# Kernel tuning notes

Hardware: AMD Instinct MI355X
Metric: run time of the kernel (lower is better)

Reference implementation:

```python
import jax, jax.numpy as jnp
import numpy as np

B, W, C, H = 2, 2048, 1024, 16
K = C // H  # 64
LN_EPS = 1e-5


def setup_inputs() -> dict:
    key = jax.random.key(0)
    ks = jax.random.split(key, 8)
    return {
        "seq1": jax.random.normal(ks[0], (B, W, C), jnp.float32),
        "seq2": jax.random.normal(ks[1], (B, W, C), jnp.float32),
        "ln_gamma": jnp.ones((C,), jnp.float32),
        "ln_beta": jnp.zeros((C,), jnp.float32),
        "q_proj": jax.random.normal(ks[2], (H, C, K), jnp.float32) * 0.02,
        "k_proj": jax.random.normal(ks[3], (H, C, K), jnp.float32) * 0.02,
        "v_proj": jax.random.normal(ks[4], (H, C, K), jnp.float32) * 0.02,
        "mixer_w": jax.random.normal(ks[5], (C, C), jnp.float32) * 0.02,
        "mixer_b": jnp.zeros((C,), jnp.float32),
    }


def _layernorm(x, gamma, beta):
    mu = jnp.mean(x, axis=-1, keepdims=True)
    var = jnp.mean(jnp.square(x - mu), axis=-1, keepdims=True)
    return (x - mu) * jax.lax.rsqrt(var + LN_EPS) * gamma + beta


def reference(seq1, seq2, ln_gamma, ln_beta, q_proj, k_proj, v_proj, mixer_w, mixer_b):
    x1 = _layernorm(seq1, ln_gamma, ln_beta)  # [B,W,C]
    x2 = _layernorm(seq2, ln_gamma, ln_beta)
    # per-head projections: [B,W,C] x [H,C,K] -> [B,H,W,K]
    q = jnp.einsum("bwc,hck->bhwk", x1, q_proj)
    k = jnp.einsum("bwc,hck->bhwk", x2, k_proj)
    v = jnp.einsum("bwc,hck->bhwk", x2, v_proj)
    scores = jnp.einsum("bhqk,bhmk->bhqm", q, k) / jnp.sqrt(jnp.float32(K))
    # causal mask (is_decoder=True)
    causal = jnp.tril(jnp.ones((W, W), bool))
    scores = jnp.where(causal[None, None], scores, jnp.float32(-jnp.inf))
    probs = jax.nn.softmax(scores, axis=-1)
    out = jnp.einsum("bhqm,bhmk->bhqk", probs, v)  # [B,H,W,K]
    out = out.transpose(0, 2, 1, 3).reshape(B, W, C)  # [B,W,C]
    return out @ mixer_w.T + mixer_b
```

## Files before the change

### kernel.cpp

```cpp
#include <hip/hip_runtime.h>
#include <math.h>

#define B_ 2
#define W_ 2048
#define C_ 1024
#define H_ 16
#define K_ 64
#define LN_EPS 1e-5f

typedef __attribute__((ext_vector_type(8))) short short8;
typedef __attribute__((ext_vector_type(4))) float float4v;

__device__ inline unsigned short f2bf(float f) {
  unsigned u = __float_as_uint(f);
  u += 0x7fffu + ((u >> 16) & 1u);
  return (unsigned short)(u >> 16);
}

__device__ __forceinline__ void gload_lds16(const short* g, short* l) {
  __builtin_amdgcn_global_load_lds(
      (const __attribute__((address_space(1))) void*)g,
      (__attribute__((address_space(3))) void*)l, 16, 0, 0);
}

__device__ inline float block_sum(float val) {
  __shared__ float sb[4];
  #pragma unroll
  for (int o = 32; o > 0; o >>= 1) val += __shfl_down(val, o, 64);
  int lane = threadIdx.x & 63, wid = threadIdx.x >> 6;
  if (lane == 0) sb[wid] = val;
  __syncthreads();
  float r = sb[0] + sb[1] + sb[2] + sb[3];
  __syncthreads();
  return r;
}

__global__ __launch_bounds__(256) void ln_kernel(
    const float* __restrict__ seq1, const float* __restrict__ seq2,
    const float* __restrict__ gamma, const float* __restrict__ beta,
    short* __restrict__ x1b, short* __restrict__ x2b) {
  int row = blockIdx.x;
  const int nrows = B_ * W_;
  bool first = row < nrows;
  const float* src = first ? seq1 : seq2;
  short* dst = first ? x1b : x2b;
  int r = first ? row : row - nrows;

  const float4* p = (const float4*)(src + (size_t)r * C_);
  float4 v = p[threadIdx.x];
  float mean = block_sum(v.x + v.y + v.z + v.w) * (1.0f / C_);
  float dx = v.x - mean, dy = v.y - mean, dz = v.z - mean, dw = v.w - mean;
  float var = block_sum(dx * dx + dy * dy + dz * dz + dw * dw) * (1.0f / C_);
  float rstd = rsqrtf(var + LN_EPS);

  float4 g = ((const float4*)gamma)[threadIdx.x];
  float4 b = ((const float4*)beta)[threadIdx.x];
  uint2 o;
  o.x = (unsigned)f2bf(dx * rstd * g.x + b.x) |
        ((unsigned)f2bf(dy * rstd * g.y + b.y) << 16);
  o.y = (unsigned)f2bf(dz * rstd * g.z + b.z) |
        ((unsigned)f2bf(dw * rstd * g.w + b.w) << 16);
  ((uint2*)(dst + (size_t)r * C_))[threadIdx.x] = o;
}

__global__ __launch_bounds__(256) void wprep_proj_kernel(
    const float* __restrict__ qp, const float* __restrict__ kp,
    const float* __restrict__ vp,
    short* __restrict__ wqt, short* __restrict__ wkt, short* __restrict__ wvt) {
  int cb = blockIdx.x, h = blockIdx.y, which = blockIdx.z;
  const float* P = (which == 0 ? qp : (which == 1 ? kp : vp)) + (size_t)h * C_ * K_;
  short* Wt = (which == 0 ? wqt : (which == 1 ? wkt : wvt));
  float scale = (which == 0) ? 0.125f : 1.0f;

  __shared__ float Ls[64][65];
  int t = threadIdx.x;
  {
    int cr = t >> 2, ks = (t & 3) * 16;
    const float* src = P + (size_t)(cb * 64 + cr) * K_ + ks;
    #pragma unroll
    for (int j = 0; j < 4; ++j) {
      float4 v = *(const float4*)(src + j * 4);
      Ls[cr][ks + j * 4 + 0] = v.x; Ls[cr][ks + j * 4 + 1] = v.y;
      Ls[cr][ks + j * 4 + 2] = v.z; Ls[cr][ks + j * 4 + 3] = v.w;
    }
  }
  __syncthreads();
  int kr = t >> 2, cs = (t & 3) * 16;
  unsigned u[8];
  #pragma unroll
  for (int i = 0; i < 8; ++i) {
    float a = Ls[cs + 2 * i][kr] * scale;
    float b = Ls[cs + 2 * i + 1][kr] * scale;
    u[i] = (unsigned)f2bf(a) | ((unsigned)f2bf(b) << 16);
  }
  short* dst = Wt + ((size_t)h * 64 + kr) * C_ + cb * 64 + cs;
  uint4 p0; p0.x = u[0]; p0.y = u[1]; p0.z = u[2]; p0.w = u[3];
  uint4 p1; p1.x = u[4]; p1.y = u[5]; p1.z = u[6]; p1.w = u[7];
  *(uint4*)dst = p0;
  *(uint4*)(dst + 8) = p1;
}

__global__ __launch_bounds__(256) void wprep_mix_kernel(
    const float* __restrict__ wm, short* __restrict__ wmb) {
  int gid = blockIdx.x * 256 + threadIdx.x;
  float4 v = ((const float4*)wm)[gid];
  uint2 o;
  o.x = (unsigned)f2bf(v.x) | ((unsigned)f2bf(v.y) << 16);
  o.y = (unsigned)f2bf(v.z) | ((unsigned)f2bf(v.w) << 16);
  ((uint2*)wmb)[gid] = o;
}

__device__ __forceinline__ void gemm_core(
    const short* __restrict__ A, const short* __restrict__ Bt,
    int arow0, int brow0, short* As, short* Bs, float4v acc[4][4]) {
  int tid = threadIdx.x;
  int wave = tid >> 6, lane = tid & 63;
  int lr = lane >> 3, lc = lane & 7;
  int sc = lc ^ lr;
  int wr = wave >> 1, wc = wave & 1;
  int lg = lane >> 4, ll = lane & 15;

  #pragma unroll
  for (int mi = 0; mi < 4; ++mi)
    #pragma unroll
    for (int ni = 0; ni < 4; ++ni) {
      acc[mi][ni][0] = 0.f; acc[mi][ni][1] = 0.f;
      acc[mi][ni][2] = 0.f; acc[mi][ni][3] = 0.f;
    }

  for (int k0 = 0; k0 < C_; k0 += 64) {
    __syncthreads();
    #pragma unroll
    for (int j = 0; j < 4; ++j) {
      int seg = wave * 4 + j;
      int r = seg * 8 + lr;
      gload_lds16(A + (size_t)(arow0 + r) * C_ + k0 + sc * 8, As + seg * 512);
      gload_lds16(Bt + (size_t)(brow0 + r) * C_ + k0 + sc * 8, Bs + seg * 512);
    }
    __syncthreads();
    #pragma unroll
    for (int kc = 0; kc < 2; ++kc) {
      int cc = kc * 4 + lg;
      short8 af[4], bf[4];
      #pragma unroll
      for (int mi = 0; mi < 4; ++mi) {
        int m = wr * 64 + mi * 16 + ll;
        af[mi] = *(const short8*)&As[m * 64 + ((cc ^ (m & 7)) << 3)];
      }
      #pragma unroll
      for (int ni = 0; ni < 4; ++ni) {
        int n = wc * 64 + ni * 16 + ll;
        bf[ni] = *(const short8*)&Bs[n * 64 + ((cc ^ (n & 7)) << 3)];
      }
      #pragma unroll
      for (int mi = 0; mi < 4; ++mi)
        #pragma unroll
        for (int ni = 0; ni < 4; ++ni)
          acc[mi][ni] = __builtin_amdgcn_mfma_f32_16x16x32_bf16(
              af[mi], bf[ni], acc[mi][ni], 0, 0, 0);
    }
  }
}

__global__ __launch_bounds__(256, 3) void gemm_qkv_kernel(
    const short* __restrict__ x1b, const short* __restrict__ x2b,
    const short* __restrict__ wqt, const short* __restrict__ wkt,
    const short* __restrict__ wvt,
    short* __restrict__ qb, short* __restrict__ kb, short* __restrict__ vtb) {
  __shared__ short As[128 * 64], Bs[128 * 64];
  int z = blockIdx.z;
  const short *A, *Bt;
  int arow0, brow0;
  if (z == 0)      { A = x1b; Bt = wqt; arow0 = blockIdx.x * 128; brow0 = blockIdx.y * 128; }
  else if (z == 1) { A = x2b; Bt = wkt; arow0 = blockIdx.x * 128; brow0 = blockIdx.y * 128; }
  else             { A = wvt; Bt = x2b; arow0 = blockIdx.y * 128; brow0 = blockIdx.x * 128; }

  float4v acc[4][4];
  gemm_core(A, Bt, arow0, brow0, As, Bs, acc);

  int wave = threadIdx.x >> 6, lane = threadIdx.x & 63;
  int wr = wave >> 1, wc = wave & 1, lg = lane >> 4, ll = lane & 15;
  if (z <= 1) {
    short* O = (z == 0) ? qb : kb;
    #pragma unroll
    for (int mi = 0; mi < 4; ++mi)
      #pragma unroll
      for (int ni = 0; ni < 4; ++ni) {
        int n = brow0 + wc * 64 + ni * 16 + ll;
        int h = n >> 6, kk = n & 63;
        #pragma unroll
        for (int r2 = 0; r2 < 4; ++r2) {
          int m = arow0 + wr * 64 + mi * 16 + lg * 4 + r2;
          int b = m >> 11, w = m & (W_ - 1);
          O[((size_t)(b * H_ + h) * W_ + w) * K_ + kk] = (short)f2bf(acc[mi][ni][r2]);
        }
      }
  } else {
    #pragma unroll
    for (int mi = 0; mi < 4; ++mi)
      #pragma unroll
      for (int ni = 0; ni < 4; ++ni) {
        int n = brow0 + wc * 64 + ni * 16 + ll;
        int b = n >> 11, w = n & (W_ - 1);
        #pragma unroll
        for (int r2 = 0; r2 < 4; ++r2) {
          int m = arow0 + wr * 64 + mi * 16 + lg * 4 + r2;
          int h = m >> 6, kk = m & 63;
          vtb[((size_t)(b * H_ + h) * K_ + kk) * W_ + w] = (short)f2bf(acc[mi][ni][r2]);
        }
      }
  }
}

__global__ __launch_bounds__(256, 3) void gemm_mix_kernel(
    const short* __restrict__ attnb, const short* __restrict__ wmb,
    const float* __restrict__ bias, float* __restrict__ out) {
  __shared__ short As[128 * 64], Bs[128 * 64];
  int arow0 = blockIdx.x * 128, brow0 = blockIdx.y * 128;
  float4v acc[4][4];
  gemm_core(attnb, wmb, arow0, brow0, As, Bs, acc);

  int wave = threadIdx.x >> 6, lane = threadIdx.x & 63;
  int wr = wave >> 1, wc = wave & 1, lg = lane >> 4, ll = lane & 15;
  #pragma unroll
  for (int mi = 0; mi < 4; ++mi)
    #pragma unroll
    for (int ni = 0; ni < 4; ++ni) {
      int n = brow0 + wc * 64 + ni * 16 + ll;
      float bv = bias[n];
      #pragma unroll
      for (int r2 = 0; r2 < 4; ++r2) {
        int m = arow0 + wr * 64 + mi * 16 + lg * 4 + r2;
        out[(size_t)m * C_ + n] = acc[mi][ni][r2] + bv;
      }
    }
}

__global__ __launch_bounds__(256, 3) void attn_mfma_kernel(
    const short* __restrict__ q, const short* __restrict__ k,
    const short* __restrict__ vt, short* __restrict__ out) {
  int bh = blockIdx.x;
  int b = bh >> 4, h = bh & 15;
  int s = blockIdx.y;
  int qt = (s < 16) ? (31 - s) : (s - 16);
  int wave = threadIdx.x >> 6;
  int lane = threadIdx.x & 63;
  int lg = lane >> 4, ll = lane & 15;

  __shared__ short Ks[2][64 * 64];
  __shared__ short Vs[2][64 * 64];
  __shared__ short Ps[4][16 * 76];

  const short* qp = q + (size_t)bh * W_ * K_;
  const short* kp = k + (size_t)bh * W_ * K_;
  const short* vb = vt + (size_t)bh * K_ * W_;

  int qrow = qt * 64 + wave * 16 + ll;
  short8 aq[2];
  #pragma unroll
  for (int kc = 0; kc < 2; ++kc)
    aq[kc] = *(const short8*)(qp + (size_t)qrow * K_ + kc * 32 + lg * 8);

  float4v o[4];
  #pragma unroll
  for (int ct = 0; ct < 4; ++ct) {
    o[ct][0] = 0.f; o[ct][1] = 0.f; o[ct][2] = 0.f; o[ct][3] = 0.f;
  }
  float m4[4], l4[4];
  #pragma unroll
  for (int r = 0; r < 4; ++r) { m4[r] = -INFINITY; l4[r] = 0.f; }

  int nkt = qt + 1;

  #define STAGE(kt, buf)                                                   \
    {                                                                      \
      const short* kbase = kp + (size_t)(kt) * 64 * K_;                    \
      const short* vbase = vb + (kt) * 64;                                 \
      _Pragma("unroll")                                                    \
      for (int j = 0; j < 2; ++j) {                                        \
        int sdx = j * 256 + (int)threadIdx.x;                              \
        int m = sdx >> 3, c7 = sdx & 7;                                    \
        int gc = c7 ^ (m & 7);                                             \
        gload_lds16(kbase + (size_t)m * K_ + gc * 8, &Ks[buf][sdx * 8]);   \
        gload_lds16(vbase + (size_t)m * W_ + gc * 8, &Vs[buf][sdx * 8]);   \
      }                                                                    \
    }

  STAGE(0, 0);
  for (int kt = 0; kt < nkt; ++kt) {
    int cur = kt & 1;
    if (kt + 1 < nkt) {
      STAGE(kt + 1, cur ^ 1);
      asm volatile("s_waitcnt vmcnt(4)\ns_barrier" ::: "memory");
    } else {
      asm volatile("s_waitcnt vmcnt(0)\ns_barrier" ::: "memory");
    }

    float4v st[4];
    #pragma unroll
    for (int nt = 0; nt < 4; ++nt) {
      st[nt][0] = 0.f; st[nt][1] = 0.f; st[nt][2] = 0.f; st[nt][3] = 0.f;
      int n = nt * 16 + ll;
      #pragma unroll
      for (int kc = 0; kc < 2; ++kc) {
        int cc = kc * 4 + lg;
        short8 bk = *(const short8*)&Ks[cur][n * 64 + ((cc ^ (n & 7)) << 3)];
        st[nt] = __builtin_amdgcn_mfma_f32_16x16x32_bf16(aq[kc], bk, st[nt], 0, 0, 0);
      }
    }
    short8 bv[4][2];
    #pragma unroll
    for (int ct = 0; ct < 4; ++ct) {
      int c = ct * 16 + ll;
      #pragma unroll
      for (int kc = 0; kc < 2; ++kc) {
        int cc = kc * 4 + lg;
        bv[ct][kc] = *(const short8*)&Vs[cur][c * 64 + ((cc ^ (c & 7)) << 3)];
      }
    }

    float sv[4][4];
    #pragma unroll
    for (int nt = 0; nt < 4; ++nt)
      #pragma unroll
      for (int r = 0; r < 4; ++r) sv[nt][r] = st[nt][r];
    if (kt == qt) {
      int rowb = qt * 64 + wave * 16 + lg * 4;
      #pragma unroll
      for (int nt = 0; nt < 4; ++nt) {
        int key = kt * 64 + nt * 16 + ll;
        #pragma unroll
        for (int r = 0; r < 4; ++r)
          if (key > rowb + r) sv[nt][r] = -INFINITY;
      }
    }
    float pv[4][4];
    #pragma unroll
    for (int r = 0; r < 4; ++r) {
      float x = fmaxf(fmaxf(sv[0][r], sv[1][r]), fmaxf(sv[2][r], sv[3][r]));
      x = fmaxf(x, __shfl_xor(x, 1, 64));
      x = fmaxf(x, __shfl_xor(x, 2, 64));
      x = fmaxf(x, __shfl_xor(x, 4, 64));
      x = fmaxf(x, __shfl_xor(x, 8, 64));
      float nm = fmaxf(m4[r], x);
      float al = __expf(m4[r] - nm);
      m4[r] = nm;
      float ps = 0.f;
      #pragma unroll
      for (int nt = 0; nt < 4; ++nt) {
        float e = __expf(sv[nt][r] - nm);
        pv[nt][r] = e;
        ps += e;
      }
      ps += __shfl_xor(ps, 1, 64);
      ps += __shfl_xor(ps, 2, 64);
      ps += __shfl_xor(ps, 4, 64);
      ps += __shfl_xor(ps, 8, 64);
      l4[r] = l4[r] * al + ps;
      #pragma unroll
      for (int ct = 0; ct < 4; ++ct) o[ct][r] *= al;
    }
    short* myP = &Ps[wave][0];
    #pragma unroll
    for (int nt = 0; nt < 4; ++nt)
      #pragma unroll
      for (int r = 0; r < 4; ++r)
        myP[(lg * 4 + r) * 76 + nt * 16 + ll] = (short)f2bf(pv[nt][r]);
    __builtin_amdgcn_s_waitcnt(0xC07F);
    short8 ap[2];
    ap[0] = *(const short8*)(myP + ll * 76 + lg * 8);
    ap[1] = *(const short8*)(myP + ll * 76 + 32 + lg * 8);
    #pragma unroll
    for (int ct = 0; ct < 4; ++ct) {
      o[ct] = __builtin_amdgcn_mfma_f32_16x16x32_bf16(ap[0], bv[ct][0], o[ct], 0, 0, 0);
      o[ct] = __builtin_amdgcn_mfma_f32_16x16x32_bf16(ap[1], bv[ct][1], o[ct], 0, 0, 0);
    }
    asm volatile("s_waitcnt lgkmcnt(0)\ns_barrier" ::: "memory");
  }
  #undef STAGE

  float inv[4];
  #pragma unroll
  for (int r = 0; r < 4; ++r) inv[r] = 1.0f / l4[r];
  #pragma unroll
  for (int ct = 0; ct < 4; ++ct)
    #pragma unroll
    for (int r = 0; r < 4; ++r) {
      int row = qt * 64 + wave * 16 + lg * 4 + r;
      out[((size_t)(b * W_ + row)) * C_ + h * K_ + ct * 16 + ll] =
          (short)f2bf(o[ct][r] * inv[r]);
    }
}

extern "C" void kernel_launch(void* const* d_in, const int* in_sizes, int n_in,
                              void* d_out, int out_size, void* d_ws, size_t ws_size,
                              hipStream_t stream) {
  const float* seq1  = (const float*)d_in[0];
  const float* seq2  = (const float*)d_in[1];
  const float* gamma = (const float*)d_in[2];
  const float* beta  = (const float*)d_in[3];
  const float* qp    = (const float*)d_in[4];
  const float* kp    = (const float*)d_in[5];
  const float* vp    = (const float*)d_in[6];
  const float* wm    = (const float*)d_in[7];
  const float* mb    = (const float*)d_in[8];
  float* out = (float*)d_out;

  char* ws = (char*)d_ws;
  const size_t NROW = (size_t)B_ * W_;
  const size_t XB = NROW * C_ * sizeof(short);
  const size_t WB = (size_t)C_ * C_ * sizeof(short);
  short* x1b = (short*)(ws);
  short* x2b = (short*)(ws + XB);
  short* qb  = (short*)(ws + 2 * XB);
  short* kb  = (short*)(ws + 3 * XB);
  short* vtb = (short*)(ws + 4 * XB);
  short* wqt = (short*)(ws + 5 * XB);
  short* wkt = (short*)(ws + 5 * XB + WB);
  short* wvt = (short*)(ws + 5 * XB + 2 * WB);
  short* wmb = (short*)(ws + 5 * XB + 3 * WB);
  short* attnb = (short*)(ws + 5 * XB + 4 * WB);

  wprep_proj_kernel<<<dim3(C_ / 64, H_, 3), dim3(256), 0, stream>>>(
      qp, kp, vp, wqt, wkt, wvt);
  wprep_mix_kernel<<<dim3(C_ * C_ / 1024), dim3(256), 0, stream>>>(wm, wmb);
  ln_kernel<<<dim3(2 * (unsigned)NROW), dim3(256), 0, stream>>>(
      seq1, seq2, gamma, beta, x1b, x2b);
  gemm_qkv_kernel<<<dim3(32, 8, 3), dim3(256), 0, stream>>>(
      x1b, x2b, wqt, wkt, wvt, qb, kb, vtb);
  attn_mfma_kernel<<<dim3(32, 32), dim3(256), 0, stream>>>(
      qb, kb, vtb, attnb);
  gemm_mix_kernel<<<dim3(32, 8), dim3(256), 0, stream>>>(attnb, wmb, mb, out);
}
```

Before: 235.0 us.

## Transpose attention MFMAs, use exp2 with folded log2e, lazy rescale softmax

```diff
diff --git a/kernel.cpp b/kernel.cpp
--- a/kernel.cpp
+++ b/kernel.cpp
@@ -10,6 +10,12 @@
 
 typedef __attribute__((ext_vector_type(8))) short short8;
 typedef __attribute__((ext_vector_type(4))) float float4v;
+
+#if __has_builtin(__builtin_amdgcn_exp2f)
+#define EXP2(x) __builtin_amdgcn_exp2f(x)
+#else
+#define EXP2(x) exp2f(x)
+#endif
 
 __device__ inline unsigned short f2bf(float f) {
   unsigned u = __float_as_uint(f);
@@ -70,7 +76,7 @@
   int cb = blockIdx.x, h = blockIdx.y, which = blockIdx.z;
   const float* P = (which == 0 ? qp : (which == 1 ? kp : vp)) + (size_t)h * C_ * K_;
   short* Wt = (which == 0 ? wqt : (which == 1 ? wkt : wvt));
-  float scale = (which == 0) ? 0.125f : 1.0f;
+  float scale = (which == 0) ? 0.125f * 1.4426950408889634f : 1.0f;
 
   __shared__ float Ls[64][65];
   int t = threadIdx.x;
@@ -249,7 +255,7 @@
 
   __shared__ short Ks[2][64 * 64];
   __shared__ short Vs[2][64 * 64];
-  __shared__ short Ps[4][16 * 76];
+  __shared__ short Ps[4][16 * 72];
 
   const short* qp = q + (size_t)bh * W_ * K_;
   const short* kp = k + (size_t)bh * W_ * K_;
@@ -266,9 +272,7 @@
   for (int ct = 0; ct < 4; ++ct) {
     o[ct][0] = 0.f; o[ct][1] = 0.f; o[ct][2] = 0.f; o[ct][3] = 0.f;
   }
-  float m4[4], l4[4];
-  #pragma unroll
-  for (int r = 0; r < 4; ++r) { m4[r] = -INFINITY; l4[r] = 0.f; }
+  float m = -INFINITY, l = 0.f;
 
   int nkt = qt + 1;
 
@@ -279,10 +283,10 @@
       _Pragma("unroll")                                                    \
       for (int j = 0; j < 2; ++j) {                                        \
         int sdx = j * 256 + (int)threadIdx.x;                              \
-        int m = sdx >> 3, c7 = sdx & 7;                                    \
-        int gc = c7 ^ (m & 7);                                             \
-        gload_lds16(kbase + (size_t)m * K_ + gc * 8, &Ks[buf][sdx * 8]);   \
-        gload_lds16(vbase + (size_t)m * W_ + gc * 8, &Vs[buf][sdx * 8]);   \
+        int mm = sdx >> 3, c7 = sdx & 7;                                   \
+        int gc = c7 ^ (mm & 7);                                            \
+        gload_lds16(kbase + (size_t)mm * K_ + gc * 8, &Ks[buf][sdx * 8]);  \
+        gload_lds16(vbase + (size_t)mm * W_ + gc * 8, &Vs[buf][sdx * 8]);  \
       }                                                                    \
     }
 
@@ -305,7 +309,7 @@
       for (int kc = 0; kc < 2; ++kc) {
         int cc = kc * 4 + lg;
         short8 bk = *(const short8*)&Ks[cur][n * 64 + ((cc ^ (n & 7)) << 3)];
-        st[nt] = __builtin_amdgcn_mfma_f32_16x16x32_bf16(aq[kc], bk, st[nt], 0, 0, 0);
+        st[nt] = __builtin_amdgcn_mfma_f32_16x16x32_bf16(bk, aq[kc], st[nt], 0, 0, 0);
       }
     }
     short8 bv[4][2];
@@ -319,77 +323,77 @@
       }
     }
 
-    float sv[4][4];
-    #pragma unroll
-    for (int nt = 0; nt < 4; ++nt)
-      #pragma unroll
-      for (int r = 0; r < 4; ++r) sv[nt][r] = st[nt][r];
     if (kt == qt) {
-      int rowb = qt * 64 + wave * 16 + lg * 4;
       #pragma unroll
       for (int nt = 0; nt < 4; ++nt) {
-        int key = kt * 64 + nt * 16 + ll;
+        int keyb = nt * 16 + lg * 4;
         #pragma unroll
         for (int r = 0; r < 4; ++r)
-          if (key > rowb + r) sv[nt][r] = -INFINITY;
-      }
-    }
-    float pv[4][4];
-    #pragma unroll
-    for (int r = 0; r < 4; ++r) {
-      float x = fmaxf(fmaxf(sv[0][r], sv[1][r]), fmaxf(sv[2][r], sv[3][r]));
-      x = fmaxf(x, __shfl_xor(x, 1, 64));
-      x = fmaxf(x, __shfl_xor(x, 2, 64));
-      x = fmaxf(x, __shfl_xor(x, 4, 64));
-      x = fmaxf(x, __shfl_xor(x, 8, 64));
-      float nm = fmaxf(m4[r], x);
-      float al = __expf(m4[r] - nm);
-      m4[r] = nm;
-      float ps = 0.f;
-      #pragma unroll
-      for (int nt = 0; nt < 4; ++nt) {
-        float e = __expf(sv[nt][r] - nm);
-        pv[nt][r] = e;
-        ps += e;
-      }
-      ps += __shfl_xor(ps, 1, 64);
-      ps += __shfl_xor(ps, 2, 64);
-      ps += __shfl_xor(ps, 4, 64);
-      ps += __shfl_xor(ps, 8, 64);
-      l4[r] = l4[r] * al + ps;
-      #pragma unroll
-      for (int ct = 0; ct < 4; ++ct) o[ct][r] *= al;
-    }
-    short* myP = &Ps[wave][0];
+          if (keyb + r > wave * 16 + ll) st[nt][r] = -INFINITY;
+      }
+    }
+
+    float mx0 = fmaxf(fmaxf(st[0][0], st[0][1]), fmaxf(st[0][2], st[0][3]));
+    float mx1 = fmaxf(fmaxf(st[1][0], st[1][1]), fmaxf(st[1][2], st[1][3]));
+    float mx2 = fmaxf(fmaxf(st[2][0], st[2][1]), fmaxf(st[2][2], st[2][3]));
+    float mx3 = fmaxf(fmaxf(st[3][0], st[3][1]), fmaxf(st[3][2], st[3][3]));
+    float lm = fmaxf(fmaxf(mx0, mx1), fmaxf(mx2, mx3));
+    lm = fmaxf(lm, __shfl_xor(lm, 16, 64));
+    lm = fmaxf(lm, __shfl_xor(lm, 32, 64));
+    if (!__all(lm <= m + 8.f)) {
+      float nm = fmaxf(m, lm);
+      float al = EXP2(m - nm);
+      m = nm;
+      l *= al;
+      #pragma unroll
+      for (int ct = 0; ct < 4; ++ct) {
+        o[ct][0] *= al; o[ct][1] *= al; o[ct][2] *= al; o[ct][3] *= al;
+      }
+    }
+    float p[4][4];
     #pragma unroll
     for (int nt = 0; nt < 4; ++nt)
       #pragma unroll
       for (int r = 0; r < 4; ++r)
-        myP[(lg * 4 + r) * 76 + nt * 16 + ll] = (short)f2bf(pv[nt][r]);
+        p[nt][r] = EXP2(st[nt][r] - m);
+    float s0 = (p[0][0] + p[0][1]) + (p[0][2] + p[0][3]);
+    float s1 = (p[1][0] + p[1][1]) + (p[1][2] + p[1][3]);
+    float s2 = (p[2][0] + p[2][1]) + (p[2][2] + p[2][3]);
+    float s3 = (p[3][0] + p[3][1]) + (p[3][2] + p[3][3]);
+    float ps = (s0 + s1) + (s2 + s3);
+    ps += __shfl_xor(ps, 16, 64);
+    ps += __shfl_xor(ps, 32, 64);
+    l += ps;
+
+    short* myP = &Ps[wave][ll * 72];
+    #pragma unroll
+    for (int nt = 0; nt < 4; ++nt) {
+      uint2 w;
+      w.x = (unsigned)f2bf(p[nt][0]) | ((unsigned)f2bf(p[nt][1]) << 16);
+      w.y = (unsigned)f2bf(p[nt][2]) | ((unsigned)f2bf(p[nt][3]) << 16);
+      *(uint2*)(myP + nt * 16 + lg * 4) = w;
+    }
     __builtin_amdgcn_s_waitcnt(0xC07F);
-    short8 ap[2];
-    ap[0] = *(const short8*)(myP + ll * 76 + lg * 8);
-    ap[1] = *(const short8*)(myP + ll * 76 + 32 + lg * 8);
+    short8 bp0 = *(const short8*)(myP + lg * 8);
+    short8 bp1 = *(const short8*)(myP + 32 + lg * 8);
     #pragma unroll
     for (int ct = 0; ct < 4; ++ct) {
-      o[ct] = __builtin_amdgcn_mfma_f32_16x16x32_bf16(ap[0], bv[ct][0], o[ct], 0, 0, 0);
-      o[ct] = __builtin_amdgcn_mfma_f32_16x16x32_bf16(ap[1], bv[ct][1], o[ct], 0, 0, 0);
+      o[ct] = __builtin_amdgcn_mfma_f32_16x16x32_bf16(bv[ct][0], bp0, o[ct], 0, 0, 0);
+      o[ct] = __builtin_amdgcn_mfma_f32_16x16x32_bf16(bv[ct][1], bp1, o[ct], 0, 0, 0);
     }
     asm volatile("s_waitcnt lgkmcnt(0)\ns_barrier" ::: "memory");
   }
   #undef STAGE
 
-  float inv[4];
-  #pragma unroll
-  for (int r = 0; r < 4; ++r) inv[r] = 1.0f / l4[r];
-  #pragma unroll
-  for (int ct = 0; ct < 4; ++ct)
-    #pragma unroll
-    for (int r = 0; r < 4; ++r) {
-      int row = qt * 64 + wave * 16 + lg * 4 + r;
-      out[((size_t)(b * W_ + row)) * C_ + h * K_ + ct * 16 + ll] =
-          (short)f2bf(o[ct][r] * inv[r]);
-    }
+  float invl = 1.0f / l;
+  size_t orow = ((size_t)(b * W_ + qrow)) * C_ + h * K_;
+  #pragma unroll
+  for (int ct = 0; ct < 4; ++ct) {
+    uint2 w;
+    w.x = (unsigned)f2bf(o[ct][0] * invl) | ((unsigned)f2bf(o[ct][1] * invl) << 16);
+    w.y = (unsigned)f2bf(o[ct][2] * invl) | ((unsigned)f2bf(o[ct][3] * invl) << 16);
+    *(uint2*)(out + orow + ct * 16 + lg * 4) = w;
+  }
 }
 
 extern "C" void kernel_launch(void* const* d_in, const int* in_sizes, int n_in,
```

Result: faster. 204.4 us (-13.0%).
